# Optimization experiments

Hardware: AMD Instinct MI355X
Metric: run time of the kernel (lower is better)

Reference implementation:

```python
import jax, jax.numpy as jnp
import numpy as np

BN_EPS = 1e-5

def _mlp(h, w1, b1, w2, b2):
    return jax.nn.relu(h @ w1 + b1) @ w2 + b2

def _segment_mean(data, seg, num_segments):
    s = jax.ops.segment_sum(data, seg, num_segments=num_segments)
    c = jax.ops.segment_sum(jnp.ones((data.shape[0],), data.dtype), seg, num_segments=num_segments)
    return s / jnp.maximum(c, 1.0)[:, None]

def _lin_init(k, fan_in, fan_out):
    k1, k2 = jax.random.split(k)
    s = 1.0 / float(np.sqrt(fan_in))
    w = jax.random.uniform(k1, (fan_in, fan_out), jnp.float32, -s, s)
    b = jax.random.uniform(k2, (fan_out,), jnp.float32, -s, s)
    return w, b

def setup_inputs() -> dict:
    key = jax.random.key(0)
    ks = jax.random.split(key, 16)
    N, E, B = 100000, 1600000, 256
    d1, d2, d3, d5, nc = 3, 50, 15, 10, 6
    x = jax.random.normal(ks[0], (N, d1), jnp.float32)
    edge_index = jax.random.randint(ks[1], (2, E), 0, N)
    edge_attr = jax.random.normal(ks[2], (E, d1), jnp.float32)
    u = jax.random.normal(ks[3], (B, 1), jnp.float32)
    batch = jnp.sort(jax.random.randint(ks[4], (N,), 0, B))
    ew1, eb1 = _lin_init(ks[5], d1 * 3, d2)
    ew2, eb2 = _lin_init(ks[6], d2, d3)
    nw1, nb1 = _lin_init(ks[7], d1 * 6, d2)
    nw2, nb2 = _lin_init(ks[8], d2, d3)
    gw1, gb1 = _lin_init(ks[9], d3 + 1, d2)
    gw2, gb2 = _lin_init(ks[10], d2, d3)
    fc1_w, fc1_b = _lin_init(ks[11], d3, d5)
    bn_g = jnp.ones((d5,), jnp.float32)
    bn_b = jnp.zeros((d5,), jnp.float32)
    fc2_w, fc2_b = _lin_init(ks[12], d5, nc)
    return dict(x=x, edge_index=edge_index, edge_attr=edge_attr, u=u, batch=batch,
                ew1=ew1, eb1=eb1, ew2=ew2, eb2=eb2,
                nw1=nw1, nb1=nb1, nw2=nw2, nb2=nb2,
                gw1=gw1, gb1=gb1, gw2=gw2, gb2=gb2,
                fc1_w=fc1_w, fc1_b=fc1_b, bn_g=bn_g, bn_b=bn_b,
                fc2_w=fc2_w, fc2_b=fc2_b)

def reference(x, edge_index, edge_attr, u, batch,
              ew1, eb1, ew2, eb2, nw1, nb1, nw2, nb2,
              gw1, gb1, gw2, gb2, fc1_w, fc1_b, bn_g, bn_b, fc2_w, fc2_b):
    N = x.shape[0]
    B = u.shape[0]
    row, col = edge_index[0], edge_index[1]
    # edge update: cat([x[row], x[col], edge_attr]) -> MLP  => [E, d3]
    e2 = _mlp(jnp.concatenate([x[row], x[col], edge_attr], axis=1), ew1, eb1, ew2, eb2)
    # node update: cat([x[col], e2]) -> MLP -> scatter_mean over row  => [N, d3]
    h = _mlp(jnp.concatenate([x[col], e2], axis=1), nw1, nb1, nw2, nb2)
    x2 = _segment_mean(h, row, N)
    # global update: cat([u, mean_per_graph(x2)]) -> MLP  => [B, d3]
    u2 = _mlp(jnp.concatenate([u, _segment_mean(x2, batch, B)], axis=1), gw1, gb1, gw2, gb2)
    # readout: relu(cat nodes + globals), mean-pool per graph (u2 rows join their graph)
    z = jax.nn.relu(jnp.concatenate([x2, u2], axis=0))  # dropout off (eval mode)
    seg = jnp.concatenate([batch, jnp.arange(B, dtype=batch.dtype)])
    g = _segment_mean(z, seg, B)  # [B, d3]
    h1 = g @ fc1_w + fc1_b
    # BatchNorm1d in eval mode with default running stats (mean=0, var=1)
    h1 = jax.nn.relu(h1 * (bn_g / jnp.sqrt(1.0 + BN_EPS)) + bn_b)
    return jax.nn.log_softmax(h1 @ fc2_w + fc2_b, axis=1)
```

## Files before the change

### kernel.cpp

```cpp
#include <hip/hip_runtime.h>
#include <math.h>

#define D1 3
#define D2 50
#define D3 15
#define D5 10
#define NC 6
#define SCAN_B 512

typedef _Float16 h2 __attribute__((ext_vector_type(2)));
typedef __fp16   fp16x2 __attribute__((ext_vector_type(2)));

__device__ __forceinline__ float fdot2(h2 a, h2 b, float c) {
#if __has_builtin(__builtin_amdgcn_fdot2)
    return __builtin_amdgcn_fdot2(a, b, c, false);
#else
    return c + (float)a[0] * (float)b[0] + (float)a[1] * (float)b[1];
#endif
}

__device__ __forceinline__ h2 pkrtz(float a, float b) {
#if __has_builtin(__builtin_amdgcn_cvt_pkrtz)
    fp16x2 r = __builtin_amdgcn_cvt_pkrtz(a, b);
    return __builtin_bit_cast(h2, r);
#else
    h2 v; v[0] = (_Float16)a; v[1] = (_Float16)b; return v;
#endif
}

__global__ __launch_bounds__(256) void deg_rank_prep_kernel(
    const int* __restrict__ ei, int* __restrict__ deg, int* __restrict__ rank, int E,
    const float* __restrict__ ew1, const float* __restrict__ nw1,
    const float* __restrict__ ew2, const float* __restrict__ nw2,
    h2* __restrict__ ew1pk, h2* __restrict__ nw1pk,
    h2* __restrict__ ew2pk, h2* __restrict__ nw2pk)
{
    int e = blockIdx.x * blockDim.x + threadIdx.x;
    if (e < E) {
        int r = ei[e];
        rank[e] = atomicAdd(&deg[r], 1);
    }
    if (blockIdx.x == 0) {
        int t = threadIdx.x;
        for (int i = t; i < D2 * 5; i += 256) {
            int j = i / 5, p = i - 5 * j;
            float a = ew1[(2 * p) * D2 + j];
            float b = (2 * p + 1 < 9) ? ew1[(2 * p + 1) * D2 + j] : 0.0f;
            h2 v; v[0] = (_Float16)a; v[1] = (_Float16)b;
            ew1pk[i] = v;
        }
        for (int i = t; i < D2 * 9; i += 256) {
            int j = i / 9, p = i - 9 * j;
            float a = nw1[(2 * p) * D2 + j];
            float b = nw1[(2 * p + 1) * D2 + j];
            h2 v; v[0] = (_Float16)a; v[1] = (_Float16)b;
            nw1pk[i] = v;
        }
        for (int i = t; i < D3 * 25; i += 256) {
            int m = i / 25, k = i - 25 * m;
            float a = ew2[(2 * k) * D3 + m];
            float b = ew2[(2 * k + 1) * D3 + m];
            h2 v; v[0] = (_Float16)a; v[1] = (_Float16)b;
            ew2pk[i] = v;
            float c = nw2[(2 * k) * D3 + m];
            float d = nw2[(2 * k + 1) * D3 + m];
            h2 w; w[0] = (_Float16)c; w[1] = (_Float16)d;
            nw2pk[i] = w;
        }
    }
}

__global__ __launch_bounds__(SCAN_B) void scan1_kernel(
    const int* __restrict__ deg, int* __restrict__ base, int* __restrict__ bsum, int N)
{
    __shared__ int sm[SCAN_B];
    int i = blockIdx.x * SCAN_B + threadIdx.x;
    int v = (i < N) ? deg[i] : 0;
    sm[threadIdx.x] = v;
    __syncthreads();
    #pragma unroll
    for (int s = 1; s < SCAN_B; s <<= 1) {
        int t = (threadIdx.x >= (unsigned)s) ? sm[threadIdx.x - s] : 0;
        __syncthreads();
        sm[threadIdx.x] += t;
        __syncthreads();
    }
    if (i < N) base[i] = sm[threadIdx.x] - v;
    if (threadIdx.x == SCAN_B - 1) bsum[blockIdx.x] = sm[threadIdx.x];
}

__global__ __launch_bounds__(SCAN_B) void scan23_kernel(
    int* __restrict__ base, const int* __restrict__ bsum, int N)
{
    int bid = blockIdx.x;
    int sum = 0;
    for (int t = (int)threadIdx.x; t < bid; t += SCAN_B) sum += bsum[t];
    #pragma unroll
    for (int s = 32; s > 0; s >>= 1) sum += __shfl_down(sum, s);
    __shared__ int ws[SCAN_B / 64];
    __shared__ int s_total;
    int lane = threadIdx.x & 63, wid = threadIdx.x >> 6;
    if (lane == 0) ws[wid] = sum;
    __syncthreads();
    if (threadIdx.x == 0) {
        int tot = 0;
        #pragma unroll
        for (int w = 0; w < SCAN_B / 64; ++w) tot += ws[w];
        s_total = tot;
    }
    __syncthreads();
    int i = bid * SCAN_B + threadIdx.x;
    if (i < N) base[i] += s_total;
}

__global__ __launch_bounds__(256, 4) void edge_mlp_fused_kernel(
    const float* __restrict__ x,
    const int*   __restrict__ ei,
    const float* __restrict__ ea,
    const h2* __restrict__ ew1pk, const float* __restrict__ eb1,
    const h2* __restrict__ ew2pk, const float* __restrict__ eb2,
    const h2* __restrict__ nw1pk, const float* __restrict__ nb1,
    const h2* __restrict__ nw2pk, const float* __restrict__ nb2,
    const int* __restrict__ base, const int* __restrict__ rank,
    unsigned int* __restrict__ hbuf16,
    int E)
{
    int e = blockIdx.x * blockDim.x + threadIdx.x;
    if (e >= E) return;

    int r = ei[e];
    int c = ei[E + e];
    int slot = base[r] + rank[e];

    float in9[9];
    in9[0] = x[3 * r + 0];
    in9[1] = x[3 * r + 1];
    in9[2] = x[3 * r + 2];
    in9[3] = x[3 * c + 0];
    in9[4] = x[3 * c + 1];
    in9[5] = x[3 * c + 2];
    in9[6] = ea[3 * (size_t)e + 0];
    in9[7] = ea[3 * (size_t)e + 1];
    in9[8] = ea[3 * (size_t)e + 2];

    h2 inpk[5];
    inpk[0] = pkrtz(in9[0], in9[1]);
    inpk[1] = pkrtz(in9[2], in9[3]);
    inpk[2] = pkrtz(in9[4], in9[5]);
    inpk[3] = pkrtz(in9[6], in9[7]);
    inpk[4] = pkrtz(in9[8], 0.0f);

    h2 hpk[25];
    #pragma unroll
    for (int jj = 0; jj < 25; ++jj) {
        float a0 = eb1[2 * jj];
        float a1 = eb1[2 * jj + 1];
        #pragma unroll
        for (int p = 0; p < 5; ++p) {
            a0 = fdot2(inpk[p], ew1pk[(2 * jj) * 5 + p], a0);
            a1 = fdot2(inpk[p], ew1pk[(2 * jj + 1) * 5 + p], a1);
        }
        hpk[jj] = pkrtz(fmaxf(a0, 0.0f), fmaxf(a1, 0.0f));
    }

    float e2v[D3];
    #pragma unroll
    for (int m = 0; m < D3; ++m) {
        float a = eb2[m];
        #pragma unroll
        for (int k = 0; k < 25; ++k) a = fdot2(hpk[k], ew2pk[m * 25 + k], a);
        e2v[m] = a;
    }

    h2 vpk[9];
    vpk[0] = pkrtz(in9[3], in9[4]);
    vpk[1] = pkrtz(in9[5], e2v[0]);
    #pragma unroll
    for (int p = 2; p < 9; ++p) vpk[p] = pkrtz(e2v[2 * p - 3], e2v[2 * p - 2]);

    h2 h2pk[25];
    #pragma unroll
    for (int jj = 0; jj < 25; ++jj) {
        float a0 = nb1[2 * jj];
        float a1 = nb1[2 * jj + 1];
        #pragma unroll
        for (int p = 0; p < 9; ++p) {
            a0 = fdot2(vpk[p], nw1pk[(2 * jj) * 9 + p], a0);
            a1 = fdot2(vpk[p], nw1pk[(2 * jj + 1) * 9 + p], a1);
        }
        h2pk[jj] = pkrtz(fmaxf(a0, 0.0f), fmaxf(a1, 0.0f));
    }

    float acc[D3 + 1];
    #pragma unroll
    for (int m = 0; m < D3; ++m) {
        float a = nb2[m];
        #pragma unroll
        for (int k = 0; k < 25; ++k) a = fdot2(h2pk[k], nw2pk[m * 25 + k], a);
        acc[m] = a;
    }
    acc[D3] = 0.0f;

    union { h2 h[8]; uint4 u[2]; } outp;
    #pragma unroll
    for (int p = 0; p < 8; ++p) outp.h[p] = pkrtz(acc[2 * p], acc[2 * p + 1]);

    uint4* dst = (uint4*)(hbuf16 + (size_t)slot * 8);
    dst[0] = outp.u[0];
    dst[1] = outp.u[1];
}

__global__ __launch_bounds__(256) void tail_kernel(
    const unsigned int* __restrict__ hbuf16,
    const int* __restrict__ deg, const int* __restrict__ base,
    const int* __restrict__ batch, int N,
    const float* __restrict__ u,
    const float* __restrict__ gw1, const float* __restrict__ gb1,
    const float* __restrict__ gw2, const float* __restrict__ gb2,
    const float* __restrict__ fc1w, const float* __restrict__ fc1b,
    const float* __restrict__ bng, const float* __restrict__ bnb,
    const float* __restrict__ fc2w, const float* __restrict__ fc2b,
    float* __restrict__ out)
{
    int b = blockIdx.x;
    int tid = threadIdx.x;

    int lo = 0, hi = N;
    while (lo < hi) { int m = (lo + hi) >> 1; if (batch[m] < b) lo = m + 1; else hi = m; }
    int start = lo;
    hi = N;
    while (lo < hi) { int m = (lo + hi) >> 1; if (batch[m] < b + 1) lo = m + 1; else hi = m; }
    int end = lo;

    float sx[D3], sr[D3];
    #pragma unroll
    for (int j = 0; j < D3; ++j) { sx[j] = 0.0f; sr[j] = 0.0f; }

    for (int i = start + tid; i < end; i += 256) {
        int bs = base[i];
        int d  = deg[i];
        float acc[16];
        #pragma unroll
        for (int j = 0; j < 16; ++j) acc[j] = 0.0f;
        const uint4* ptr = (const uint4*)(hbuf16 + (size_t)bs * 8);
        for (int k = 0; k < d; ++k) {
            uint4 w0 = ptr[2 * k];
            uint4 w1 = ptr[2 * k + 1];
            unsigned int ws[8] = {w0.x, w0.y, w0.z, w0.w, w1.x, w1.y, w1.z, w1.w};
            #pragma unroll
            for (int p = 0; p < 8; ++p) {
                h2 v = __builtin_bit_cast(h2, ws[p]);
                acc[2 * p]     += (float)v[0];
                acc[2 * p + 1] += (float)v[1];
            }
        }
        float inv = 1.0f / fmaxf((float)d, 1.0f);
        #pragma unroll
        for (int j = 0; j < D3; ++j) {
            float v = acc[j] * inv;
            sx[j] += v;
            sr[j] += fmaxf(v, 0.0f);
        }
    }

    #pragma unroll
    for (int j = 0; j < D3; ++j) {
        #pragma unroll
        for (int s = 32; s > 0; s >>= 1) {
            sx[j] += __shfl_down(sx[j], s);
            sr[j] += __shfl_down(sr[j], s);
        }
    }

    __shared__ float sm[4][2 * D3];
    __shared__ float s_red[2 * D3];
    __shared__ float s_in16[16];
    __shared__ float s_gh[D2];
    __shared__ float s_g[D3];
    __shared__ float s_h1[D5];

    int lane = tid & 63, wid = tid >> 6;
    if (lane == 0) {
        #pragma unroll
        for (int j = 0; j < D3; ++j) { sm[wid][j] = sx[j]; sm[wid][D3 + j] = sr[j]; }
    }
    __syncthreads();

    float nct = (float)(end - start);

    if (tid < 2 * D3) {
        s_red[tid] = sm[0][tid] + sm[1][tid] + sm[2][tid] + sm[3][tid];
    }
    __syncthreads();

    if (tid < 16) {
        s_in16[tid] = (tid == 0) ? u[b] : s_red[tid - 1] / fmaxf(nct, 1.0f);
    }
    __syncthreads();

    if (tid < D2) {
        float a = gb1[tid];
        #pragma unroll
        for (int k = 0; k < 16; ++k) a = fmaf(s_in16[k], gw1[k * D2 + tid], a);
        s_gh[tid] = fmaxf(a, 0.0f);
    }
    __syncthreads();

    if (tid < D3) {
        float a = gb2[tid];
        #pragma unroll
        for (int k = 0; k < D2; ++k) a = fmaf(s_gh[k], gw2[k * D3 + tid], a);
        s_g[tid] = (s_red[D3 + tid] + fmaxf(a, 0.0f)) / (nct + 1.0f);
    }
    __syncthreads();

    if (tid < D5) {
        const float bnscale = 1.0f / sqrtf(1.0f + 1e-5f);
        float a = fc1b[tid];
        #pragma unroll
        for (int k = 0; k < D3; ++k) a = fmaf(s_g[k], fc1w[k * D5 + tid], a);
        s_h1[tid] = fmaxf(a * (bng[tid] * bnscale) + bnb[tid], 0.0f);
    }
    __syncthreads();

    if (tid == 0) {
        float o[NC];
        #pragma unroll
        for (int j = 0; j < NC; ++j) {
            float a = fc2b[j];
            #pragma unroll
            for (int k = 0; k < D5; ++k) a = fmaf(s_h1[k], fc2w[k * NC + j], a);
            o[j] = a;
        }
        float m = o[0];
        #pragma unroll
        for (int j = 1; j < NC; ++j) m = fmaxf(m, o[j]);
        float ssum = 0.0f;
        #pragma unroll
        for (int j = 0; j < NC; ++j) ssum += expf(o[j] - m);
        float lse = m + logf(ssum);
        #pragma unroll
        for (int j = 0; j < NC; ++j) out[b * NC + j] = o[j] - lse;
    }
}

__global__ __launch_bounds__(256) void edge_node_atomic_kernel(
    const float* __restrict__ x,
    const int*   __restrict__ ei,
    const float* __restrict__ ea,
    const float* __restrict__ ew1, const float* __restrict__ eb1,
    const float* __restrict__ ew2, const float* __restrict__ eb2,
    const float* __restrict__ nw1, const float* __restrict__ nb1,
    const float* __restrict__ nw2, const float* __restrict__ nb2,
    float* __restrict__ x2sum, float* __restrict__ cnt,
    int E)
{
    int e = blockIdx.x * blockDim.x + threadIdx.x;
    if (e >= E) return;
    int r = ei[e];
    int c = ei[E + e];
    float in9[9];
    in9[0] = x[3 * r + 0]; in9[1] = x[3 * r + 1]; in9[2] = x[3 * r + 2];
    float xc0 = x[3 * c + 0], xc1 = x[3 * c + 1], xc2 = x[3 * c + 2];
    in9[3] = xc0; in9[4] = xc1; in9[5] = xc2;
    in9[6] = ea[3 * e + 0]; in9[7] = ea[3 * e + 1]; in9[8] = ea[3 * e + 2];
    float h[D2];
    #pragma unroll
    for (int j = 0; j < D2; ++j) {
        float a = eb1[j];
        #pragma unroll
        for (int k = 0; k < 9; ++k) a = fmaf(in9[k], ew1[k * D2 + j], a);
        h[j] = fmaxf(a, 0.0f);
    }
    float e2[D3];
    #pragma unroll
    for (int j = 0; j < D3; ++j) {
        float a = eb2[j];
        #pragma unroll
        for (int k = 0; k < D2; ++k) a = fmaf(h[k], ew2[k * D3 + j], a);
        e2[j] = a;
    }
    float h2v[D2];
    #pragma unroll
    for (int j = 0; j < D2; ++j) {
        float a = nb1[j];
        a = fmaf(xc0, nw1[0 * D2 + j], a);
        a = fmaf(xc1, nw1[1 * D2 + j], a);
        a = fmaf(xc2, nw1[2 * D2 + j], a);
        #pragma unroll
        for (int k = 0; k < D3; ++k) a = fmaf(e2[k], nw1[(3 + k) * D2 + j], a);
        h2v[j] = fmaxf(a, 0.0f);
    }
    float* dst = x2sum + (size_t)r * D3;
    #pragma unroll
    for (int j = 0; j < D3; ++j) {
        float a = nb2[j];
        #pragma unroll
        for (int k = 0; k < D2; ++k) a = fmaf(h2v[k], nw2[k * D3 + j], a);
        atomicAdd(&dst[j], a);
    }
    atomicAdd(&cnt[r], 1.0f);
}

__global__ __launch_bounds__(256) void graph_sum_atomic_kernel(
    const float* __restrict__ x2sum, const float* __restrict__ cnt,
    const int* __restrict__ batch, int N,
    float* __restrict__ bx, float* __restrict__ brelu, float* __restrict__ ncnt)
{
    int b = blockIdx.x;
    int lo = 0, hi = N;
    while (lo < hi) { int m = (lo + hi) >> 1; if (batch[m] < b) lo = m + 1; else hi = m; }
    int start = lo;
    hi = N;
    while (lo < hi) { int m = (lo + hi) >> 1; if (batch[m] < b + 1) lo = m + 1; else hi = m; }
    int end = lo;
    float sx[D3], sr[D3];
    #pragma unroll
    for (int j = 0; j < D3; ++j) { sx[j] = 0.0f; sr[j] = 0.0f; }
    for (int i = start + (int)threadIdx.x; i < end; i += (int)blockDim.x) {
        float inv = 1.0f / fmaxf(cnt[i], 1.0f);
        #pragma unroll
        for (int j = 0; j < D3; ++j) {
            float v = x2sum[(size_t)i * D3 + j] * inv;
            sx[j] += v;
            sr[j] += fmaxf(v, 0.0f);
        }
    }
    #pragma unroll
    for (int j = 0; j < D3; ++j) {
        #pragma unroll
        for (int s = 32; s > 0; s >>= 1) {
            sx[j] += __shfl_down(sx[j], s);
            sr[j] += __shfl_down(sr[j], s);
        }
    }
    __shared__ float sm[4][2 * D3];
    int lane = threadIdx.x & 63, wid = threadIdx.x >> 6;
    if (lane == 0) {
        #pragma unroll
        for (int j = 0; j < D3; ++j) { sm[wid][j] = sx[j]; sm[wid][D3 + j] = sr[j]; }
    }
    __syncthreads();
    if (threadIdx.x < 2 * D3) {
        float v = sm[0][threadIdx.x] + sm[1][threadIdx.x] + sm[2][threadIdx.x] + sm[3][threadIdx.x];
        if (threadIdx.x < D3) bx[b * D3 + threadIdx.x] = v;
        else                  brelu[b * D3 + (threadIdx.x - D3)] = v;
    }
    if (threadIdx.x == 0) ncnt[b] = (float)(end - start);
}

__global__ __launch_bounds__(256) void final_kernel(
    const float* __restrict__ u,
    const float* __restrict__ gw1, const float* __restrict__ gb1,
    const float* __restrict__ gw2, const float* __restrict__ gb2,
    const float* __restrict__ fc1w, const float* __restrict__ fc1b,
    const float* __restrict__ bng, const float* __restrict__ bnb,
    const float* __restrict__ fc2w, const float* __restrict__ fc2b,
    const float* __restrict__ bx, const float* __restrict__ brelu,
    const float* __restrict__ ncnt,
    float* __restrict__ out, int B)
{
    int t = blockIdx.x * blockDim.x + threadIdx.x;
    if (t >= B) return;
    float nct = ncnt[t];
    float inv = 1.0f / fmaxf(nct, 1.0f);
    float in16[16];
    in16[0] = u[t];
    #pragma unroll
    for (int j = 0; j < D3; ++j) in16[1 + j] = bx[t * D3 + j] * inv;
    float gh[D2];
    #pragma unroll
    for (int j = 0; j < D2; ++j) {
        float a = gb1[j];
        #pragma unroll
        for (int k = 0; k < 16; ++k) a = fmaf(in16[k], gw1[k * D2 + j], a);
        gh[j] = fmaxf(a, 0.0f);
    }
    float g[D3];
    #pragma unroll
    for (int j = 0; j < D3; ++j) {
        float a = gb2[j];
        #pragma unroll
        for (int k = 0; k < D2; ++k) a = fmaf(gh[k], gw2[k * D3 + j], a);
        g[j] = (brelu[t * D3 + j] + fmaxf(a, 0.0f)) / (nct + 1.0f);
    }
    const float bnscale = 1.0f / sqrtf(1.0f + 1e-5f);
    float h1[D5];
    #pragma unroll
    for (int i = 0; i < D5; ++i) {
        float a = fc1b[i];
        #pragma unroll
        for (int k = 0; k < D3; ++k) a = fmaf(g[k], fc1w[k * D5 + i], a);
        h1[i] = fmaxf(a * (bng[i] * bnscale) + bnb[i], 0.0f);
    }
    float o[NC];
    #pragma unroll
    for (int j = 0; j < NC; ++j) {
        float a = fc2b[j];
        #pragma unroll
        for (int k = 0; k < D5; ++k) a = fmaf(h1[k], fc2w[k * NC + j], a);
        o[j] = a;
    }
    float m = o[0];
    #pragma unroll
    for (int j = 1; j < NC; ++j) m = fmaxf(m, o[j]);
    float ssum = 0.0f;
    #pragma unroll
    for (int j = 0; j < NC; ++j) ssum += expf(o[j] - m);
    float lse = m + logf(ssum);
    #pragma unroll
    for (int j = 0; j < NC; ++j) out[t * NC + j] = o[j] - lse;
}

extern "C" void kernel_launch(void* const* d_in, const int* in_sizes, int n_in,
                              void* d_out, int out_size, void* d_ws, size_t ws_size,
                              hipStream_t stream) {
    const float* x     = (const float*)d_in[0];
    const int*   ei    = (const int*)  d_in[1];
    const float* ea    = (const float*)d_in[2];
    const float* u     = (const float*)d_in[3];
    const int*   batch = (const int*)  d_in[4];
    const float* ew1 = (const float*)d_in[5];
    const float* eb1 = (const float*)d_in[6];
    const float* ew2 = (const float*)d_in[7];
    const float* eb2 = (const float*)d_in[8];
    const float* nw1 = (const float*)d_in[9];
    const float* nb1 = (const float*)d_in[10];
    const float* nw2 = (const float*)d_in[11];
    const float* nb2 = (const float*)d_in[12];
    const float* gw1 = (const float*)d_in[13];
    const float* gb1 = (const float*)d_in[14];
    const float* gw2 = (const float*)d_in[15];
    const float* gb2 = (const float*)d_in[16];
    const float* fc1w = (const float*)d_in[17];
    const float* fc1b = (const float*)d_in[18];
    const float* bng  = (const float*)d_in[19];
    const float* bnb  = (const float*)d_in[20];
    const float* fc2w = (const float*)d_in[21];
    const float* fc2b = (const float*)d_in[22];

    int N = in_sizes[0] / 3;
    int E = in_sizes[2] / 3;
    int B = in_sizes[3];
    float* out = (float*)d_out;

    int nsb = (N + SCAN_B - 1) / SCAN_B;
    const size_t WPK = 2048;

    size_t need = sizeof(h2) * WPK
                + sizeof(unsigned int) * (size_t)E * 8
                + sizeof(int) * ((size_t)N + (size_t)E + (size_t)N + 1024);

    if (ws_size >= need && nsb <= 1024) {
        char* p = (char*)d_ws;
        h2* ew1pk = (h2*)p;
        h2* nw1pk = ew1pk + 250;
        h2* ew2pk = nw1pk + 450;
        h2* nw2pk = ew2pk + 375;
        p += sizeof(h2) * WPK;
        unsigned int* hbuf16 = (unsigned int*)p;  p += sizeof(unsigned int) * (size_t)E * 8;
        int* deg  = (int*)p;            p += sizeof(int) * (size_t)N;
        int* rank = (int*)p;            p += sizeof(int) * (size_t)E;
        int* base = (int*)p;            p += sizeof(int) * (size_t)N;
        int* bsum = (int*)p;            p += sizeof(int) * 1024;

        hipMemsetAsync(deg, 0, sizeof(int) * (size_t)N, stream);

        int eb = (E + 255) / 256;
        deg_rank_prep_kernel<<<eb, 256, 0, stream>>>(
            ei, deg, rank, E, ew1, nw1, ew2, nw2, ew1pk, nw1pk, ew2pk, nw2pk);

        scan1_kernel<<<nsb, SCAN_B, 0, stream>>>(deg, base, bsum, N);
        scan23_kernel<<<nsb, SCAN_B, 0, stream>>>(base, bsum, N);

        edge_mlp_fused_kernel<<<eb, 256, 0, stream>>>(
            x, ei, ea, ew1pk, eb1, ew2pk, eb2, nw1pk, nb1, nw2pk, nb2,
            base, rank, hbuf16, E);

        tail_kernel<<<B, 256, 0, stream>>>(
            hbuf16, deg, base, batch, N,
            u, gw1, gb1, gw2, gb2, fc1w, fc1b, bng, bnb, fc2w, fc2b, out);
    } else {
        float* x2sum = (float*)d_ws;
        float* cnt   = x2sum + (size_t)N * D3;
        float* bx    = cnt + N;
        float* brelu = bx + (size_t)B * D3;
        float* ncnt  = brelu + (size_t)B * D3;

        hipMemsetAsync(x2sum, 0, sizeof(float) * ((size_t)N * D3 + N), stream);

        int eb = (E + 255) / 256;
        edge_node_atomic_kernel<<<eb, 256, 0, stream>>>(
            x, ei, ea, ew1, eb1, ew2, eb2, nw1, nb1, nw2, nb2, x2sum, cnt, E);

        graph_sum_atomic_kernel<<<B, 256, 0, stream>>>(x2sum, cnt, batch, N, bx, brelu, ncnt);

        int fb = (B + 255) / 256;
        final_kernel<<<fb, 256, 0, stream>>>(
            u, gw1, gb1, gw2, gb2, fc1w, fc1b, bng, bnb, fc2w, fc2b,
            bx, brelu, ncnt, out, B);
    }
}
```

Measured before the change: 206.2 us.

## Compute per-edge MLPs with MFMA 16x16x32 f16 tiles per wavefront

Replaces the per-thread fdot2 edge and node MLP chain with wavefront-level MFMA matrix multiplies. Each wave handles 16 edges and stages activations through LDS to transpose between layers, and a grid-stride loop is capped at 1024 blocks. Weights are pre-packed into MFMA B-operand fragments held in registers. This removes most scalar dot-product ALU work, but adds LDS round-trips, zero-padding waste (K=9 padded to 32), and only one lane group does the gathers.

```diff
diff --git a/kernel.cpp b/kernel.cpp
--- a/kernel.cpp
+++ b/kernel.cpp
@@ -1,7 +1,6 @@
 #include <hip/hip_runtime.h>
 #include <math.h>
 
-#define D1 3
 #define D2 50
 #define D3 15
 #define D5 10
@@ -9,31 +8,14 @@
 #define SCAN_B 512
 
 typedef _Float16 h2 __attribute__((ext_vector_type(2)));
-typedef __fp16   fp16x2 __attribute__((ext_vector_type(2)));
-
-__device__ __forceinline__ float fdot2(h2 a, h2 b, float c) {
-#if __has_builtin(__builtin_amdgcn_fdot2)
-    return __builtin_amdgcn_fdot2(a, b, c, false);
-#else
-    return c + (float)a[0] * (float)b[0] + (float)a[1] * (float)b[1];
-#endif
-}
-
-__device__ __forceinline__ h2 pkrtz(float a, float b) {
-#if __has_builtin(__builtin_amdgcn_cvt_pkrtz)
-    fp16x2 r = __builtin_amdgcn_cvt_pkrtz(a, b);
-    return __builtin_bit_cast(h2, r);
-#else
-    h2 v; v[0] = (_Float16)a; v[1] = (_Float16)b; return v;
-#endif
-}
+typedef _Float16 f16x8 __attribute__((ext_vector_type(8)));
+typedef float    f32x4 __attribute__((ext_vector_type(4)));
 
 __global__ __launch_bounds__(256) void deg_rank_prep_kernel(
     const int* __restrict__ ei, int* __restrict__ deg, int* __restrict__ rank, int E,
     const float* __restrict__ ew1, const float* __restrict__ nw1,
     const float* __restrict__ ew2, const float* __restrict__ nw2,
-    h2* __restrict__ ew1pk, h2* __restrict__ nw1pk,
-    h2* __restrict__ ew2pk, h2* __restrict__ nw2pk)
+    _Float16* __restrict__ wBf)
 {
     int e = blockIdx.x * blockDim.x + threadIdx.x;
     if (e < E) {
@@ -41,31 +23,30 @@
         rank[e] = atomicAdd(&deg[r], 1);
     }
     if (blockIdx.x == 0) {
-        int t = threadIdx.x;
-        for (int i = t; i < D2 * 5; i += 256) {
-            int j = i / 5, p = i - 5 * j;
-            float a = ew1[(2 * p) * D2 + j];
-            float b = (2 * p + 1 < 9) ? ew1[(2 * p + 1) * D2 + j] : 0.0f;
-            h2 v; v[0] = (_Float16)a; v[1] = (_Float16)b;
-            ew1pk[i] = v;
-        }
-        for (int i = t; i < D2 * 9; i += 256) {
-            int j = i / 9, p = i - 9 * j;
-            float a = nw1[(2 * p) * D2 + j];
-            float b = nw1[(2 * p + 1) * D2 + j];
-            h2 v; v[0] = (_Float16)a; v[1] = (_Float16)b;
-            nw1pk[i] = v;
-        }
-        for (int i = t; i < D3 * 25; i += 256) {
-            int m = i / 25, k = i - 25 * m;
-            float a = ew2[(2 * k) * D3 + m];
-            float b = ew2[(2 * k + 1) * D3 + m];
-            h2 v; v[0] = (_Float16)a; v[1] = (_Float16)b;
-            ew2pk[i] = v;
-            float c = nw2[(2 * k) * D3 + m];
-            float d = nw2[(2 * k + 1) * D3 + m];
-            h2 w; w[0] = (_Float16)c; w[1] = (_Float16)d;
-            nw2pk[i] = w;
+        for (int q = threadIdx.x; q < 12 * 64 * 8; q += 256) {
+            int i = q & 7;
+            int l = (q >> 3) & 63;
+            int t = q >> 9;
+            int col = l & 15, grp = l >> 4;
+            int k = grp * 8 + i;
+            float v = 0.0f;
+            if (t < 4) {
+                int n = t * 16 + col;
+                if (k < 9 && n < D2) v = ew1[k * D2 + n];
+            } else if (t < 6) {
+                int kk = (t - 4) * 32 + k;
+                if (kk < D2 && col < D3) v = ew2[kk * D3 + col];
+            } else if (t < 10) {
+                int n = (t - 6) * 16 + col;
+                if (n < D2) {
+                    if (k < 15)      v = nw1[(3 + k) * D2 + n];
+                    else if (k < 18) v = nw1[(k - 15) * D2 + n];
+                }
+            } else {
+                int kk = (t - 10) * 32 + k;
+                if (kk < D2 && col < D3) v = nw2[kk * D3 + col];
+            }
+            wBf[q] = (_Float16)v;
         }
     }
 }
@@ -113,101 +94,148 @@
     if (i < N) base[i] += s_total;
 }
 
-__global__ __launch_bounds__(256, 4) void edge_mlp_fused_kernel(
+__global__ __launch_bounds__(256) void edge_mlp_mfma_kernel(
     const float* __restrict__ x,
     const int*   __restrict__ ei,
     const float* __restrict__ ea,
-    const h2* __restrict__ ew1pk, const float* __restrict__ eb1,
-    const h2* __restrict__ ew2pk, const float* __restrict__ eb2,
-    const h2* __restrict__ nw1pk, const float* __restrict__ nb1,
-    const h2* __restrict__ nw2pk, const float* __restrict__ nb2,
+    const f16x8* __restrict__ wB,
+    const float* __restrict__ eb1, const float* __restrict__ eb2,
+    const float* __restrict__ nb1, const float* __restrict__ nb2,
     const int* __restrict__ base, const int* __restrict__ rank,
     unsigned int* __restrict__ hbuf16,
-    int E)
-{
-    int e = blockIdx.x * blockDim.x + threadIdx.x;
-    if (e >= E) return;
-
-    int r = ei[e];
-    int c = ei[E + e];
-    int slot = base[r] + rank[e];
-
-    float in9[9];
-    in9[0] = x[3 * r + 0];
-    in9[1] = x[3 * r + 1];
-    in9[2] = x[3 * r + 2];
-    in9[3] = x[3 * c + 0];
-    in9[4] = x[3 * c + 1];
-    in9[5] = x[3 * c + 2];
-    in9[6] = ea[3 * (size_t)e + 0];
-    in9[7] = ea[3 * (size_t)e + 1];
-    in9[8] = ea[3 * (size_t)e + 2];
-
-    h2 inpk[5];
-    inpk[0] = pkrtz(in9[0], in9[1]);
-    inpk[1] = pkrtz(in9[2], in9[3]);
-    inpk[2] = pkrtz(in9[4], in9[5]);
-    inpk[3] = pkrtz(in9[6], in9[7]);
-    inpk[4] = pkrtz(in9[8], 0.0f);
-
-    h2 hpk[25];
-    #pragma unroll
-    for (int jj = 0; jj < 25; ++jj) {
-        float a0 = eb1[2 * jj];
-        float a1 = eb1[2 * jj + 1];
-        #pragma unroll
-        for (int p = 0; p < 5; ++p) {
-            a0 = fdot2(inpk[p], ew1pk[(2 * jj) * 5 + p], a0);
-            a1 = fdot2(inpk[p], ew1pk[(2 * jj + 1) * 5 + p], a1);
-        }
-        hpk[jj] = pkrtz(fmaxf(a0, 0.0f), fmaxf(a1, 0.0f));
-    }
-
-    float e2v[D3];
-    #pragma unroll
-    for (int m = 0; m < D3; ++m) {
-        float a = eb2[m];
-        #pragma unroll
-        for (int k = 0; k < 25; ++k) a = fdot2(hpk[k], ew2pk[m * 25 + k], a);
-        e2v[m] = a;
-    }
-
-    h2 vpk[9];
-    vpk[0] = pkrtz(in9[3], in9[4]);
-    vpk[1] = pkrtz(in9[5], e2v[0]);
-    #pragma unroll
-    for (int p = 2; p < 9; ++p) vpk[p] = pkrtz(e2v[2 * p - 3], e2v[2 * p - 2]);
-
-    h2 h2pk[25];
-    #pragma unroll
-    for (int jj = 0; jj < 25; ++jj) {
-        float a0 = nb1[2 * jj];
-        float a1 = nb1[2 * jj + 1];
-        #pragma unroll
-        for (int p = 0; p < 9; ++p) {
-            a0 = fdot2(vpk[p], nw1pk[(2 * jj) * 9 + p], a0);
-            a1 = fdot2(vpk[p], nw1pk[(2 * jj + 1) * 9 + p], a1);
-        }
-        h2pk[jj] = pkrtz(fmaxf(a0, 0.0f), fmaxf(a1, 0.0f));
-    }
-
-    float acc[D3 + 1];
-    #pragma unroll
-    for (int m = 0; m < D3; ++m) {
-        float a = nb2[m];
-        #pragma unroll
-        for (int k = 0; k < 25; ++k) a = fdot2(h2pk[k], nw2pk[m * 25 + k], a);
-        acc[m] = a;
-    }
-    acc[D3] = 0.0f;
-
-    union { h2 h[8]; uint4 u[2]; } outp;
-    #pragma unroll
-    for (int p = 0; p < 8; ++p) outp.h[p] = pkrtz(acc[2 * p], acc[2 * p + 1]);
-
-    uint4* dst = (uint4*)(hbuf16 + (size_t)slot * 8);
-    dst[0] = outp.u[0];
-    dst[1] = outp.u[1];
+    int E, int ngroups)
+{
+    __shared__ _Float16 tr[4][16][72];
+    __shared__ int slotbuf[4][16];
+
+    int tid  = threadIdx.x;
+    int lane = tid & 63;
+    int wid  = tid >> 6;
+    int col  = lane & 15;
+    int grp  = lane >> 4;
+
+    f16x8 wf[12];
+    #pragma unroll
+    for (int t = 0; t < 12; ++t) wf[t] = wB[t * 64 + lane];
+
+    float be1v[4], bn1v[4];
+    #pragma unroll
+    for (int t = 0; t < 4; ++t) {
+        int n = t * 16 + col;
+        be1v[t] = (n < D2) ? eb1[n] : 0.0f;
+        bn1v[t] = (n < D2) ? nb1[n] : 0.0f;
+    }
+    float be2v = (col < D3) ? eb2[col] : 0.0f;
+    float bn2v = (col < D3) ? nb2[col] : 0.0f;
+
+    int gw = blockIdx.x * 4 + wid;
+    int nw = gridDim.x * 4;
+
+    for (int g = gw; g < ngroups; g += nw) {
+        int e0 = g * 16;
+        int e  = e0 + col;
+        int ec = (e < E) ? e : (E - 1);
+
+        f16x8 a1;
+        #pragma unroll
+        for (int i = 0; i < 8; ++i) a1[i] = (_Float16)0.0f;
+        float xc0 = 0.0f, xc1 = 0.0f, xc2 = 0.0f;
+
+        if (grp == 0) {
+            int r = ei[ec], c = ei[E + ec];
+            slotbuf[wid][col] = (e < E) ? (base[r] + rank[ec]) : -1;
+            float xr0 = x[3 * r], xr1 = x[3 * r + 1], xr2 = x[3 * r + 2];
+            xc0 = x[3 * c]; xc1 = x[3 * c + 1]; xc2 = x[3 * c + 2];
+            float ea0 = ea[3 * (size_t)ec], ea1 = ea[3 * (size_t)ec + 1];
+            a1[0] = (_Float16)xr0; a1[1] = (_Float16)xr1; a1[2] = (_Float16)xr2;
+            a1[3] = (_Float16)xc0; a1[4] = (_Float16)xc1; a1[5] = (_Float16)xc2;
+            a1[6] = (_Float16)ea0; a1[7] = (_Float16)ea1;
+        } else if (grp == 1) {
+            a1[0] = (_Float16)ea[3 * (size_t)ec + 2];
+        }
+
+        f32x4 hacc[4];
+        #pragma unroll
+        for (int t = 0; t < 4; ++t) {
+            f32x4 cin = {be1v[t], be1v[t], be1v[t], be1v[t]};
+            hacc[t] = __builtin_amdgcn_mfma_f32_16x16x32_f16(a1, wf[t], cin, 0, 0, 0);
+        }
+        #pragma unroll
+        for (int t = 0; t < 4; ++t) {
+            int n = t * 16 + col;
+            #pragma unroll
+            for (int r2 = 0; r2 < 4; ++r2) {
+                int eidx = grp * 4 + r2;
+                float v = (n < D2) ? fmaxf(hacc[t][r2], 0.0f) : 0.0f;
+                tr[wid][eidx][n] = (_Float16)v;
+            }
+        }
+
+        f16x8 alo = *(const f16x8*)&tr[wid][col][grp * 8];
+        f16x8 ahi = *(const f16x8*)&tr[wid][col][32 + grp * 8];
+        f32x4 e2acc = {be2v, be2v, be2v, be2v};
+        e2acc = __builtin_amdgcn_mfma_f32_16x16x32_f16(alo, wf[4], e2acc, 0, 0, 0);
+        e2acc = __builtin_amdgcn_mfma_f32_16x16x32_f16(ahi, wf[5], e2acc, 0, 0, 0);
+
+        #pragma unroll
+        for (int r2 = 0; r2 < 4; ++r2) {
+            int eidx = grp * 4 + r2;
+            if (col < D3) tr[wid][eidx][col] = (_Float16)e2acc[r2];
+        }
+        if (grp == 0) {
+            tr[wid][col][15] = (_Float16)xc0;
+            tr[wid][col][16] = (_Float16)xc1;
+            tr[wid][col][17] = (_Float16)xc2;
+        }
+        #pragma unroll
+        for (int pass = 0; pass < 2; ++pass) {
+            int zz = lane + pass * 64;
+            if (zz < 112) {
+                int eidx = zz / 7, sl = zz % 7;
+                *((unsigned int*)&tr[wid][eidx][18 + sl * 2]) = 0u;
+            }
+        }
+
+        f16x8 an = *(const f16x8*)&tr[wid][col][grp * 8];
+        f32x4 h2acc[4];
+        #pragma unroll
+        for (int t = 0; t < 4; ++t) {
+            f32x4 cin = {bn1v[t], bn1v[t], bn1v[t], bn1v[t]};
+            h2acc[t] = __builtin_amdgcn_mfma_f32_16x16x32_f16(an, wf[6 + t], cin, 0, 0, 0);
+        }
+        #pragma unroll
+        for (int t = 0; t < 4; ++t) {
+            int n = t * 16 + col;
+            #pragma unroll
+            for (int r2 = 0; r2 < 4; ++r2) {
+                int eidx = grp * 4 + r2;
+                float v = (n < D2) ? fmaxf(h2acc[t][r2], 0.0f) : 0.0f;
+                tr[wid][eidx][n] = (_Float16)v;
+            }
+        }
+
+        alo = *(const f16x8*)&tr[wid][col][grp * 8];
+        ahi = *(const f16x8*)&tr[wid][col][32 + grp * 8];
+        f32x4 oacc = {bn2v, bn2v, bn2v, bn2v};
+        oacc = __builtin_amdgcn_mfma_f32_16x16x32_f16(alo, wf[10], oacc, 0, 0, 0);
+        oacc = __builtin_amdgcn_mfma_f32_16x16x32_f16(ahi, wf[11], oacc, 0, 0, 0);
+
+        #pragma unroll
+        for (int r2 = 0; r2 < 4; ++r2) {
+            int eidx = grp * 4 + r2;
+            if (col < D3) tr[wid][eidx][col] = (_Float16)oacc[r2];
+            else          tr[wid][eidx][15]  = (_Float16)0.0f;
+        }
+
+        if (lane < 32) {
+            int eidx = lane >> 1, half = lane & 1;
+            int slot = slotbuf[wid][eidx];
+            if (slot >= 0) {
+                uint4 v = *(const uint4*)&tr[wid][eidx][half * 8];
+                *(uint4*)(hbuf16 + (size_t)slot * 8 + half * 4) = v;
+            }
+        }
+    }
 }
 
 __global__ __launch_bounds__(256) void tail_kernel(
@@ -545,19 +573,15 @@
     float* out = (float*)d_out;
 
     int nsb = (N + SCAN_B - 1) / SCAN_B;
-    const size_t WPK = 2048;
-
-    size_t need = sizeof(h2) * WPK
+    const size_t WBF = 12 * 64 * 8;
+
+    size_t need = sizeof(_Float16) * WBF
                 + sizeof(unsigned int) * (size_t)E * 8
                 + sizeof(int) * ((size_t)N + (size_t)E + (size_t)N + 1024);
 
     if (ws_size >= need && nsb <= 1024) {
         char* p = (char*)d_ws;
-        h2* ew1pk = (h2*)p;
-        h2* nw1pk = ew1pk + 250;
-        h2* ew2pk = nw1pk + 450;
-        h2* nw2pk = ew2pk + 375;
-        p += sizeof(h2) * WPK;
+        _Float16* wBf = (_Float16*)p;       p += sizeof(_Float16) * WBF;
         unsigned int* hbuf16 = (unsigned int*)p;  p += sizeof(unsigned int) * (size_t)E * 8;
         int* deg  = (int*)p;            p += sizeof(int) * (size_t)N;
         int* rank = (int*)p;            p += sizeof(int) * (size_t)E;
@@ -568,14 +592,17 @@
 
         int eb = (E + 255) / 256;
         deg_rank_prep_kernel<<<eb, 256, 0, stream>>>(
-            ei, deg, rank, E, ew1, nw1, ew2, nw2, ew1pk, nw1pk, ew2pk, nw2pk);
+            ei, deg, rank, E, ew1, nw1, ew2, nw2, wBf);
 
         scan1_kernel<<<nsb, SCAN_B, 0, stream>>>(deg, base, bsum, N);
         scan23_kernel<<<nsb, SCAN_B, 0, stream>>>(base, bsum, N);
 
-        edge_mlp_fused_kernel<<<eb, 256, 0, stream>>>(
-            x, ei, ea, ew1pk, eb1, ew2pk, eb2, nw1pk, nb1, nw2pk, nb2,
-            base, rank, hbuf16, E);
+        int ngroups = (E + 15) / 16;
+        int nb = (ngroups + 3) / 4;
+        if (nb > 1024) nb = 1024;
+        edge_mlp_mfma_kernel<<<nb, 256, 0, stream>>>(
+            x, ei, ea, (const f16x8*)wBf, eb1, eb2, nb1, nb2,
+            base, rank, hbuf16, E, ngroups);
 
         tail_kernel<<<B, 256, 0, stream>>>(
             hbuf16, deg, base, batch, N,
```

Result: slower. 224.0 us (+8.6%).
